# Kernel tuning notes

Measured on AMD Instinct MI355X. Metric: run time of the kernel, lower is better.

The kernel has to match this reference:

```python
import jax, jax.numpy as jnp
import numpy as np

B, L, NW, H, HID, E, NL, DL = 32, 1024, 512, 768, 384, 4, 12, 128


def setup_inputs() -> dict:
    key = jax.random.key(0)
    ks = jax.random.split(key, 16)
    f = lambda k, s: jax.random.normal(k, s, dtype=jnp.float32) * 0.02
    z = lambda s: jnp.zeros(s, jnp.float32)
    return {
        "token_embs": jax.random.normal(ks[0], (B, L, H), dtype=jnp.float32),
        "word_maps": jnp.sort(jax.random.randint(ks[1], (B, L), 0, NW), axis=-1),
        "lang_ids": jax.random.randint(ks[2], (B,), 0, NL),
        # BiLSTM params (PyTorch gate order i,f,g,o packed along dim 0)
        "Wih_f": f(ks[3], (4 * HID, H)), "Whh_f": f(ks[4], (4 * HID, HID)),
        "bih_f": z((4 * HID,)), "bhh_f": z((4 * HID,)),
        "Wih_b": f(ks[5], (4 * HID, H)), "Whh_b": f(ks[6], (4 * HID, HID)),
        "bih_b": z((4 * HID,)), "bhh_b": z((4 * HID,)),
        "proj_W": f(ks[7], (H, 2 * HID)), "proj_b": z((H,)),
        "lang_table": f(ks[8], (NL, DL)),
        "gate_W1": f(ks[9], (H, H + DL)), "gate_b1": z((H,)),
        "gate_W2": f(ks[10], (E, H)), "gate_b2": z((E,)),
        # stacked expert heads: row i is expert i's (H,1) linear
        "ef_W": f(ks[11], (E, H)), "ef_b": z((E,)),
        "ed_W": f(ks[12], (E, H)), "ed_b": z((E,)),
    }


def _seg_mean(embs, wmap):
    # embs: [L, H], wmap: [L] -> [NW, H] per-word mean of subword embeddings
    sums = jax.ops.segment_sum(embs, wmap, num_segments=NW)
    cnt = jax.ops.segment_sum(jnp.ones(embs.shape[:1], embs.dtype), wmap, num_segments=NW)
    return sums / jnp.maximum(cnt, 1.0)[:, None]


def _lstm(x, Wih, Whh, bih, bhh, reverse):
    # x: [B, T, H] -> hidden states [B, T, HID]; gate order i,f,g,o
    def step(carry, xg):
        h, c = carry
        g = xg + h @ Whh.T + bhh
        i, fg, gg, o = jnp.split(g, 4, axis=-1)
        c = jax.nn.sigmoid(fg) * c + jax.nn.sigmoid(i) * jnp.tanh(gg)
        h = jax.nn.sigmoid(o) * jnp.tanh(c)
        return (h, c), h
    xg = jnp.swapaxes(x @ Wih.T + bih, 0, 1)  # [T, B, 4*HID], input proj hoisted
    init = (jnp.zeros((x.shape[0], Whh.shape[1]), x.dtype),) * 2
    _, hs = jax.lax.scan(step, init, xg, reverse=reverse)
    return jnp.swapaxes(hs, 0, 1)


def reference(token_embs, word_maps, lang_ids, Wih_f, Whh_f, bih_f, bhh_f,
              Wih_b, Whh_b, bih_b, bhh_b, proj_W, proj_b, lang_table,
              gate_W1, gate_b1, gate_W2, gate_b2, ef_W, ef_b, ed_W, ed_b):
    # subword -> word segment-mean pooling, batched
    word_embs = jax.vmap(_seg_mean)(token_embs, word_maps)          # [B, NW, H]
    hf = _lstm(word_embs, Wih_f, Whh_f, bih_f, bhh_f, False)        # [B, NW, HID]
    hb = _lstm(word_embs, Wih_b, Whh_b, bih_b, bhh_b, True)         # [B, NW, HID]
    seq = jnp.concatenate([hf, hb], axis=-1) @ proj_W.T + proj_b    # [B, NW, H]
    # dropout omitted (eval mode)
    gate_in = jnp.concatenate([token_embs[:, 0], lang_table[lang_ids]], axis=-1)  # [B, H+DL]
    gate = jax.nn.softmax(
        jax.nn.relu(gate_in @ gate_W1.T + gate_b1) @ gate_W2.T + gate_b2, axis=-1)  # [B, E]
    fix = jnp.einsum('bwe,be->bw', seq @ ef_W.T + ef_b, gate)       # [B, NW]
    dur = jnp.einsum('bwe,be->bw', seq @ ed_W.T + ed_b, gate)       # [B, NW]
    return (fix, dur)
```

## Files before the change

kernel.cpp:

```cpp
#include <hip/hip_runtime.h>
#include <stdint.h>

#define BB 32
#define LL 1024
#define NW 512
#define HH 768
#define HID 384
#define G4 1536
#define EE 4
#define DLL 128
#define GIN 896
#define CWG 12
#define WGC 32
#define HPAD 392

typedef __attribute__((ext_vector_type(8))) short short8;
typedef __attribute__((ext_vector_type(4))) float f32x4;
typedef __attribute__((ext_vector_type(4))) unsigned int u32x4;
typedef __attribute__((ext_vector_type(2))) unsigned int u32x2;

__device__ __forceinline__ float bf2f(short s){
  union { unsigned int u; float f; } v; v.u = ((unsigned int)(unsigned short)s) << 16; return v.f;
}
__device__ __forceinline__ short f2bf(float f){
  union { float f; unsigned int u; } v; v.f = f;
  unsigned int r = v.u + 0x7fffu + ((v.u >> 16) & 1u);
  return (short)(r >> 16);
}
__device__ __forceinline__ float sigm(float x){ return 1.f / (1.f + __expf(-x)); }
__device__ __forceinline__ float ftanh(float x){ float e = __expf(2.f * x); return 1.f - 2.f / (e + 1.f); }

__device__ __forceinline__ void gload16(const void* g, void* l){
  __builtin_amdgcn_global_load_lds(
      (const __attribute__((address_space(1))) unsigned int*)g,
      (__attribute__((address_space(3))) unsigned int*)l, 16, 0, 0);
}

__global__ void k_f2bf(const float* in, short* out, int n){
  int i = blockIdx.x * blockDim.x + threadIdx.x;
  int st = gridDim.x * blockDim.x;
  for (; i < n; i += st) out[i] = f2bf(in[i]);
}

__global__ __launch_bounds__(256) void k_segmean(const float* __restrict__ tok,
                                                 const int* __restrict__ wmap,
                                                 short* __restrict__ we_bf){
  int blk = blockIdx.x;
  int b = blk >> 9;
  int w = blk & 511;
  const int* m = wmap + b * LL;
  int lo = 0, hi = LL;
  while (lo < hi){ int mid = (lo + hi) >> 1; if (m[mid] < w) lo = mid + 1; else hi = mid; }
  int s = lo;
  int lo2 = s, hi2 = LL;
  while (lo2 < hi2){ int mid = (lo2 + hi2) >> 1; if (m[mid] <= w) lo2 = mid + 1; else hi2 = mid; }
  int e = lo2;
  float cnt = (float)(e - s);
  float denom = fmaxf(cnt, 1.f);
  for (int j = threadIdx.x; j < HH; j += 256){
    float acc = 0.f;
    for (int r = s; r < e; ++r) acc += tok[((size_t)b * LL + r) * HH + j];
    we_bf[((size_t)b * NW + w) * HH + j] = f2bf(acc / denom);
  }
}

__global__ __launch_bounds__(256) void k_gemm_bt(const short* __restrict__ Abf,
                                                 const short* __restrict__ Wbf,
                                                 const float* __restrict__ b1,
                                                 const float* __restrict__ b2,
                                                 float* __restrict__ Cf,
                                                 int M, int N, int K){
  __shared__ __attribute__((aligned(16))) short As[128 * 32];
  __shared__ __attribute__((aligned(16))) short Bs[128 * 32];
  int ntiles = N >> 7;
  int m0 = (blockIdx.x / ntiles) << 7;
  int n0 = (blockIdx.x % ntiles) << 7;
  int tid = threadIdx.x, lane = tid & 63, wv = tid >> 6;
  int wm = (wv >> 1) << 6, wn = (wv & 1) << 6;
  f32x4 acc[4][4] = {};
  for (int kk = 0; kk < K; kk += 32){
#pragma unroll
    for (int q = 0; q < 2; ++q){
      int e = q * 256 + tid;
      int row = e >> 2, col = (e & 3) << 3;
      gload16(Abf + (size_t)(m0 + row) * K + kk + col, As + e * 8);
      gload16(Wbf + (size_t)(n0 + row) * K + kk + col, Bs + e * 8);
    }
    __syncthreads();
    short8 af[4], bfr[4];
#pragma unroll
    for (int x = 0; x < 4; ++x){
      af[x]  = *(const short8*)(As + (wm + x * 16 + (lane & 15)) * 32 + ((lane >> 4) << 3));
      bfr[x] = *(const short8*)(Bs + (wn + x * 16 + (lane & 15)) * 32 + ((lane >> 4) << 3));
    }
#pragma unroll
    for (int x = 0; x < 4; ++x)
#pragma unroll
      for (int y = 0; y < 4; ++y)
        acc[x][y] = __builtin_amdgcn_mfma_f32_16x16x32_bf16(af[x], bfr[y], acc[x][y], 0, 0, 0);
    __syncthreads();
  }
#pragma unroll
  for (int x = 0; x < 4; ++x)
#pragma unroll
    for (int y = 0; y < 4; ++y)
#pragma unroll
      for (int i = 0; i < 4; ++i){
        int mm = m0 + wm + x * 16 + ((lane >> 4) << 2) + i;
        int nn = n0 + wn + y * 16 + (lane & 15);
        Cf[(size_t)mm * N + nn] = acc[x][y][i] + b1[nn] + b2[nn];
      }
}

__global__ __launch_bounds__(512) void k_lstm(const float* __restrict__ xg_f,
                                              const float* __restrict__ xg_b,
                                              const short* __restrict__ whh_f,
                                              const short* __restrict__ whh_b,
                                              unsigned int* __restrict__ hbuf,
                                              short* __restrict__ hcat){
  int bx = blockIdx.x;
  int dir = bx / CWG;
  int cg  = bx % CWG;
  int tid = threadIdx.x, lane = tid & 63, wv = tid >> 6;
  int q = lane >> 4, fr = lane & 15;
  int g = wv >> 1, nh = wv & 1;
  int jbase = g * HID + cg * WGC + nh * 16;
  const float* xg  = dir ? xg_b : xg_f;
  const short* whh = dir ? whh_b : whh_f;

  short8 bfrag[12];
  {
    const short* wr = whh + (size_t)(jbase + fr) * HID + q * 8;
#pragma unroll
    for (int ks = 0; ks < 12; ++ks) bfrag[ks] = *(const short8*)(wr + ks * 32);
  }

  __shared__ __attribute__((aligned(16))) short hs[2][16 * HPAD];
  __shared__ float pre[4][16][34];

  float cst0 = 0.f, cst1 = 0.f;
  int eb = tid >> 5, ecol = tid & 31;
  int sc = (tid & 31) * 12;
  unsigned int* hbD = hbuf + (size_t)dir * 2 * 2 * 16 * HID;

  float nxg[4];
  {
    int t0a = dir ? (NW - 1) : 0;
    const float* xp = xg + (size_t)t0a * G4 + jbase + fr;
#pragma unroll
    for (int i = 0; i < 4; ++i)
      nxg[i] = xp[(size_t)(q * 4 + i) * NW * G4];
  }
  u32x4 d0, d1, d2;
  const unsigned int* hp_sav = hbD;

  for (int tt = 0; tt < 2 * NW; ++tt){
    int X = tt & 1, t = tt >> 1;
    int t_act = dir ? (NW - 1 - t) : t;
    asm volatile("s_waitcnt vmcnt(0)" ::: "memory");
    __builtin_amdgcn_sched_barrier(0);
    if (t > 0){
      unsigned int expect = (unsigned int)t & 0xffffu;
      for (;;){
#define TAGBAD(dv) (((dv[0] ^ expect) | (dv[1] ^ expect) | (dv[2] ^ expect) | (dv[3] ^ expect)) & 0xffffu)
        unsigned int bad = TAGBAD(d0) | TAGBAD(d1) | TAGBAD(d2);
#undef TAGBAD
        if (__all(bad == 0)) break;
        __builtin_amdgcn_s_sleep(1);
        asm volatile("global_load_dwordx4 %0, %1, off sc0 sc1" : "=v"(d0) : "v"(hp_sav + 0) : "memory");
        asm volatile("global_load_dwordx4 %0, %1, off sc0 sc1" : "=v"(d1) : "v"(hp_sav + 4) : "memory");
        asm volatile("global_load_dwordx4 %0, %1, off sc0 sc1" : "=v"(d2) : "v"(hp_sav + 8) : "memory");
        asm volatile("s_waitcnt vmcnt(0)" ::: "memory");
        __builtin_amdgcn_sched_barrier(0);
      }
      unsigned int pk0 = (d0[0] >> 16) | (d0[1] & 0xffff0000u);
      unsigned int pk1 = (d0[2] >> 16) | (d0[3] & 0xffff0000u);
      unsigned int pk2 = (d1[0] >> 16) | (d1[1] & 0xffff0000u);
      unsigned int pk3 = (d1[2] >> 16) | (d1[3] & 0xffff0000u);
      unsigned int pk4 = (d2[0] >> 16) | (d2[1] & 0xffff0000u);
      unsigned int pk5 = (d2[2] >> 16) | (d2[3] & 0xffff0000u);
      short* dst = &hs[X][eb * HPAD + sc];
      u32x2 w0 = {pk0, pk1}, w1 = {pk2, pk3}, w2 = {pk4, pk5};
      *(u32x2*)(dst)     = w0;
      *(u32x2*)(dst + 4) = w1;
      *(u32x2*)(dst + 8) = w2;
      if (cg == 0){
        int tprev = dir ? (NW - t) : (t - 1);
        short* dh = hcat + ((size_t)(X * 16 + eb) * NW + tprev) * HH + dir * HID + sc;
        *(u32x2*)(dh)     = w0;
        *(u32x2*)(dh + 4) = w1;
        *(u32x2*)(dh + 8) = w2;
      }
    }
    asm volatile("s_waitcnt lgkmcnt(0)" ::: "memory");
    __builtin_amdgcn_s_barrier();
    __builtin_amdgcn_sched_barrier(0);
    f32x4 acc = {}, accB = {};
    if (t > 0){
      const short* hrow = &hs[X][fr * HPAD + q * 8];
#pragma unroll
      for (int ks = 0; ks < 6; ++ks)
        acc  = __builtin_amdgcn_mfma_f32_16x16x32_bf16(*(const short8*)(hrow + ks * 32), bfrag[ks], acc, 0, 0, 0);
#pragma unroll
      for (int ks = 6; ks < 12; ++ks)
        accB = __builtin_amdgcn_mfma_f32_16x16x32_bf16(*(const short8*)(hrow + ks * 32), bfrag[ks], accB, 0, 0, 0);
      acc += accB;
    }
#pragma unroll
    for (int i = 0; i < 4; ++i)
      pre[g][q * 4 + i][nh * 16 + fr] = acc[i] + nxg[i];
    __builtin_amdgcn_sched_barrier(0);
    if (tt + 1 < 2 * NW){
      int Xn = 1 - X, tn = X ? (t + 1) : t;
      int tna = dir ? (NW - 1 - tn) : tn;
      const float* xp = xg + ((size_t)(Xn * 16) * NW + tna) * G4 + jbase + fr;
#pragma unroll
      for (int i = 0; i < 4; ++i)
        nxg[i] = xp[(size_t)(q * 4 + i) * NW * G4];
      if (tn > 0){
        hp_sav = hbD + ((size_t)Xn * 2 + ((tn - 1) & 1)) * 16 * HID + eb * HID + sc;
        asm volatile("global_load_dwordx4 %0, %1, off sc0 sc1" : "=v"(d0) : "v"(hp_sav + 0) : "memory");
        asm volatile("global_load_dwordx4 %0, %1, off sc0 sc1" : "=v"(d1) : "v"(hp_sav + 4) : "memory");
        asm volatile("global_load_dwordx4 %0, %1, off sc0 sc1" : "=v"(d2) : "v"(hp_sav + 8) : "memory");
      }
    }
    asm volatile("s_waitcnt lgkmcnt(0)" ::: "memory");
    __builtin_amdgcn_s_barrier();
    __builtin_amdgcn_sched_barrier(0);
    float gi2 = pre[0][eb][ecol], gf2 = pre[1][eb][ecol];
    float gg2 = pre[2][eb][ecol], go2 = pre[3][eb][ecol];
    float c = X ? cst1 : cst0;
    c = sigm(gf2) * c + sigm(gi2) * ftanh(gg2);
    float h = sigm(go2) * ftanh(c);
    if (X) cst1 = c; else cst0 = c;
    unsigned int hv = (unsigned int)(unsigned short)f2bf(h);
    unsigned int wtag = (hv << 16) | ((unsigned int)(t + 1) & 0xffffu);
    unsigned int* hw = hbD + ((size_t)X * 2 + (t & 1)) * 16 * HID + eb * HID + cg * WGC + ecol;
    asm volatile("global_store_dword %0, %1, off sc0 sc1" :: "v"(hw), "v"(wtag) : "memory");
    if (t == NW - 1)
      hcat[((size_t)(X * 16 + eb) * NW + t_act) * HH + dir * HID + cg * WGC + ecol] = (short)hv;
  }
}

__global__ __launch_bounds__(256) void k_gate(const float* __restrict__ tok,
                                              const int* __restrict__ lids,
                                              const float* __restrict__ ltab,
                                              const float* __restrict__ W1,
                                              const float* __restrict__ b1v,
                                              const float* __restrict__ W2,
                                              const float* __restrict__ b2v,
                                              float* __restrict__ gate){
  __shared__ float gin[GIN];
  __shared__ float hid[HH];
  __shared__ float pr[EE];
  int b = blockIdx.x, tid = threadIdx.x;
  int lid = lids[b];
  for (int i = tid; i < GIN; i += 256)
    gin[i] = (i < HH) ? tok[(size_t)b * LL * HH + i] : ltab[lid * DLL + (i - HH)];
  __syncthreads();
  for (int j = tid; j < HH; j += 256){
    float a = b1v[j];
    const float* wr = W1 + (size_t)j * GIN;
    for (int k = 0; k < GIN; ++k) a += gin[k] * wr[k];
    hid[j] = fmaxf(a, 0.f);
  }
  __syncthreads();
  int wv = tid >> 6, lane = tid & 63;
  if (wv < EE){
    float p = 0.f;
    for (int k = lane; k < HH; k += 64) p += hid[k] * W2[wv * HH + k];
#pragma unroll
    for (int off = 32; off; off >>= 1) p += __shfl_down(p, off);
    if (lane == 0) pr[wv] = p + b2v[wv];
  }
  __syncthreads();
  if (tid == 0){
    float mx = fmaxf(fmaxf(pr[0], pr[1]), fmaxf(pr[2], pr[3]));
    float s = 0.f, ex[EE];
    for (int e2 = 0; e2 < EE; ++e2){ ex[e2] = __expf(pr[e2] - mx); s += ex[e2]; }
    for (int e2 = 0; e2 < EE; ++e2) gate[b * EE + e2] = ex[e2] / s;
  }
}

__global__ __launch_bounds__(256) void k_headpre(const float* __restrict__ efW,
                                                 const float* __restrict__ efb,
                                                 const float* __restrict__ edW,
                                                 const float* __restrict__ edb,
                                                 const float* __restrict__ projW,
                                                 const float* __restrict__ projb,
                                                 float* __restrict__ Acomb,
                                                 float* __restrict__ Ccomb){
  int head = blockIdx.x >> 2, e2 = blockIdx.x & 3, tid = threadIdx.x;
  const float* Wv = head ? edW : efW;
  const float* bv = head ? edb : efb;
  __shared__ float wrow[HH];
  for (int i = tid; i < HH; i += 256) wrow[i] = Wv[e2 * HH + i];
  __syncthreads();
  for (int c = tid; c < HH; c += 256){
    float a = 0.f;
    for (int h2 = 0; h2 < HH; ++h2) a += wrow[h2] * projW[(size_t)h2 * HH + c];
    Acomb[(head * 4 + e2) * HH + c] = a;
  }
  int wv = tid >> 6, lane = tid & 63;
  if (wv == 0){
    float p = 0.f;
    for (int k = lane; k < HH; k += 64) p += wrow[k] * projb[k];
#pragma unroll
    for (int off = 32; off; off >>= 1) p += __shfl_down(p, off);
    if (lane == 0) Ccomb[head * 4 + e2] = p + bv[e2];
  }
}

__global__ __launch_bounds__(256) void k_heads(const short* __restrict__ hcat,
                                               const float* __restrict__ Acomb,
                                               const float* __restrict__ Ccomb,
                                               const float* __restrict__ gate,
                                               float* __restrict__ outp){
  __shared__ float Al[8 * HH];
  int tid = threadIdx.x;
  for (int i = tid; i < 8 * HH; i += 256) Al[i] = Acomb[i];
  __syncthreads();
  int wv = tid >> 6, lane = tid & 63;
  int bw = blockIdx.x * 4 + wv;
  const short* hr = hcat + (size_t)bw * HH;
  float hv[12];
#pragma unroll
  for (int j = 0; j < 12; ++j) hv[j] = bf2f(hr[lane + 64 * j]);
  float dsum[8];
#pragma unroll
  for (int v = 0; v < 8; ++v){
    float p = 0.f;
#pragma unroll
    for (int j = 0; j < 12; ++j) p += hv[j] * Al[v * HH + lane + 64 * j];
#pragma unroll
    for (int off = 32; off; off >>= 1) p += __shfl_xor(p, off);
    dsum[v] = p;
  }
  if (lane == 0){
    int b = bw >> 9;
    float fx = 0.f, du = 0.f;
#pragma unroll
    for (int e2 = 0; e2 < 4; ++e2){
      float g = gate[b * 4 + e2];
      fx += g * (dsum[e2]     + Ccomb[e2]);
      du += g * (dsum[4 + e2] + Ccomb[4 + e2]);
    }
    outp[bw] = fx;
    outp[BB * NW + bw] = du;
  }
}

extern "C" void kernel_launch(void* const* d_in, const int* in_sizes, int n_in,
                              void* d_out, int out_size, void* d_ws, size_t ws_size,
                              hipStream_t stream){
  const float* tok   = (const float*)d_in[0];
  const int*   wmap  = (const int*)d_in[1];
  const int*   lids  = (const int*)d_in[2];
  const float* Wih_f = (const float*)d_in[3];
  const float* Whh_f = (const float*)d_in[4];
  const float* bih_f = (const float*)d_in[5];
  const float* bhh_f = (const float*)d_in[6];
  const float* Wih_b = (const float*)d_in[7];
  const float* Whh_b = (const float*)d_in[8];
  const float* bih_b = (const float*)d_in[9];
  const float* bhh_b = (const float*)d_in[10];
  const float* projW = (const float*)d_in[11];
  const float* projb = (const float*)d_in[12];
  const float* ltab  = (const float*)d_in[13];
  const float* gW1   = (const float*)d_in[14];
  const float* gb1   = (const float*)d_in[15];
  const float* gW2   = (const float*)d_in[16];
  const float* gb2   = (const float*)d_in[17];
  const float* efW   = (const float*)d_in[18];
  const float* efb   = (const float*)d_in[19];
  const float* edW   = (const float*)d_in[20];
  const float* edb   = (const float*)d_in[21];
  float* outp = (float*)d_out;

  char* ws = (char*)d_ws;
  size_t off = 0;
  auto alloc = [&](size_t bytes) -> char* {
    char* p = ws + off;
    off = (off + bytes + 255) & ~(size_t)255;
    return p;
  };
  short* we_bf   = (short*)alloc((size_t)BB * NW * HH * 2);
  short* wihf_bf = (short*)alloc((size_t)G4 * HH * 2);
  short* wihb_bf = (short*)alloc((size_t)G4 * HH * 2);
  short* whhf_bf = (short*)alloc((size_t)G4 * HID * 2);
  short* whhb_bf = (short*)alloc((size_t)G4 * HID * 2);
  float* xg_f    = (float*)alloc((size_t)BB * NW * G4 * 4);
  float* xg_b    = (float*)alloc((size_t)BB * NW * G4 * 4);
  short* hcat    = (short*)alloc((size_t)BB * NW * HH * 2);
  unsigned int* hbuf = (unsigned int*)alloc((size_t)2 * 2 * 2 * 16 * HID * 4);
  float* gateb   = (float*)alloc((size_t)BB * EE * 4);
  float* Acomb   = (float*)alloc((size_t)8 * HH * 4);
  float* Ccomb   = (float*)alloc((size_t)8 * 4);

  k_f2bf<<<1024, 256, 0, stream>>>(Wih_f, wihf_bf, G4 * HH);
  k_f2bf<<<1024, 256, 0, stream>>>(Wih_b, wihb_bf, G4 * HH);
  k_f2bf<<<512, 256, 0, stream>>>(Whh_f, whhf_bf, G4 * HID);
  k_f2bf<<<512, 256, 0, stream>>>(Whh_b, whhb_bf, G4 * HID);
  k_segmean<<<BB * NW, 256, 0, stream>>>(tok, wmap, we_bf);
  k_gemm_bt<<<(BB * NW / 128) * (G4 / 128), 256, 0, stream>>>(we_bf, wihf_bf, bih_f, bhh_f, xg_f, BB * NW, G4, HH);
  k_gemm_bt<<<(BB * NW / 128) * (G4 / 128), 256, 0, stream>>>(we_bf, wihb_bf, bih_b, bhh_b, xg_b, BB * NW, G4, HH);
  k_gate<<<BB, 256, 0, stream>>>(tok, lids, ltab, gW1, gb1, gW2, gb2, gateb);
  k_headpre<<<8, 256, 0, stream>>>(efW, efb, edW, edb, projW, projb, Acomb, Ccomb);
  k_lstm<<<2 * CWG, 512, 0, stream>>>(xg_f, xg_b, whhf_bf, whhb_bf, hbuf, hcat);
  k_heads<<<(BB * NW) / 4, 256, 0, stream>>>(hcat, Acomb, Ccomb, gateb, outp);
}
```

Before: 2.378 ms.

## Unroll LSTM recurrence over two batch halves with counted vmcnt prefetching

The LSTM recurrence loop is manually unrolled into two explicit half-steps, one per batch half (A/B), each with its own hidden-state buffer and x-gate registers. Global loads now go through inline asm, and partial s_waitcnt vmcnt counts replace the full vmcnt(0) drain, so that one half's h exchange and xg prefetch stay in flight while the other half computes. The final step skips the tagged exchange store and writes hcat directly. The cost is hand-maintained wait counts that must match the exact issue order; a wrong count could read data before it arrives.

New measurement: 2.075 ms. 1.15x faster.

```diff
diff --git a/kernel.cpp b/kernel.cpp
--- a/kernel.cpp
+++ b/kernel.cpp
@@ -112,6 +112,8 @@
       }
 }
 
+#define TAGBAD(dv) (((dv[0] ^ expect) | (dv[1] ^ expect) | (dv[2] ^ expect) | (dv[3] ^ expect)) & 0xffffu)
+
 __global__ __launch_bounds__(512) void k_lstm(const float* __restrict__ xg_f,
                                               const float* __restrict__ xg_b,
                                               const short* __restrict__ whh_f,
@@ -132,113 +134,208 @@
   {
     const short* wr = whh + (size_t)(jbase + fr) * HID + q * 8;
 #pragma unroll
-    for (int ks = 0; ks < 12; ++ks) bfrag[ks] = *(const short8*)(wr + ks * 32);
+    for (int ks = 0; ks < 12; ++ks)
+      asm volatile("global_load_dwordx4 %0, %1, off" : "=v"(bfrag[ks]) : "v"(wr + ks * 32) : "memory");
+    asm volatile("s_waitcnt vmcnt(0)" ::: "memory");
+    __builtin_amdgcn_sched_barrier(0);
   }
 
   __shared__ __attribute__((aligned(16))) short hs[2][16 * HPAD];
   __shared__ float pre[4][16][34];
 
-  float cst0 = 0.f, cst1 = 0.f;
+  float cA = 0.f, cB = 0.f;
   int eb = tid >> 5, ecol = tid & 31;
   int sc = (tid & 31) * 12;
   unsigned int* hbD = hbuf + (size_t)dir * 2 * 2 * 16 * HID;
-
-  float nxg[4];
+  const size_t RS = (size_t)NW * G4;
+
+  float xa0, xa1, xa2, xa3, xb0, xb1, xb2, xb3;
+  u32x4 dA0, dA1, dA2, dB0, dB1, dB2;
+
   {
-    int t0a = dir ? (NW - 1) : 0;
-    const float* xp = xg + (size_t)t0a * G4 + jbase + fr;
-#pragma unroll
-    for (int i = 0; i < 4; ++i)
-      nxg[i] = xp[(size_t)(q * 4 + i) * NW * G4];
-  }
-  u32x4 d0, d1, d2;
-  const unsigned int* hp_sav = hbD;
-
-  for (int tt = 0; tt < 2 * NW; ++tt){
-    int X = tt & 1, t = tt >> 1;
-    int t_act = dir ? (NW - 1 - t) : t;
-    asm volatile("s_waitcnt vmcnt(0)" ::: "memory");
-    __builtin_amdgcn_sched_barrier(0);
-    if (t > 0){
-      unsigned int expect = (unsigned int)t & 0xffffu;
+    int ta = dir ? (NW - 1) : 0;
+    const float* xpA = xg + (size_t)ta * G4 + jbase + fr;
+    asm volatile("global_load_dword %0, %1, off" : "=v"(xa0) : "v"(xpA + (size_t)(q*4+0)*RS) : "memory");
+    asm volatile("global_load_dword %0, %1, off" : "=v"(xa1) : "v"(xpA + (size_t)(q*4+1)*RS) : "memory");
+    asm volatile("global_load_dword %0, %1, off" : "=v"(xa2) : "v"(xpA + (size_t)(q*4+2)*RS) : "memory");
+    asm volatile("global_load_dword %0, %1, off" : "=v"(xa3) : "v"(xpA + (size_t)(q*4+3)*RS) : "memory");
+    const float* xpB = xpA + (size_t)16 * RS;
+    asm volatile("global_load_dword %0, %1, off" : "=v"(xb0) : "v"(xpB + (size_t)(q*4+0)*RS) : "memory");
+    asm volatile("global_load_dword %0, %1, off" : "=v"(xb1) : "v"(xpB + (size_t)(q*4+1)*RS) : "memory");
+    asm volatile("global_load_dword %0, %1, off" : "=v"(xb2) : "v"(xpB + (size_t)(q*4+2)*RS) : "memory");
+    asm volatile("global_load_dword %0, %1, off" : "=v"(xb3) : "v"(xpB + (size_t)(q*4+3)*RS) : "memory");
+  }
+
+  for (int j = 0; j < NW; ++j){
+    int t_act = dir ? (NW - 1 - j) : j;
+    if (j == 0) { asm volatile("s_waitcnt vmcnt(4)" ::: "memory"); }
+    else        { asm volatile("s_waitcnt vmcnt(5)" ::: "memory"); }
+    __builtin_amdgcn_sched_barrier(0);
+    if (j > 0){
+      unsigned int expect = (unsigned int)j & 0xffffu;
+      const unsigned int* hpr = hbD + (size_t)((j - 1) & 1) * 16 * HID + eb * HID + sc;
       for (;;){
-#define TAGBAD(dv) (((dv[0] ^ expect) | (dv[1] ^ expect) | (dv[2] ^ expect) | (dv[3] ^ expect)) & 0xffffu)
-        unsigned int bad = TAGBAD(d0) | TAGBAD(d1) | TAGBAD(d2);
-#undef TAGBAD
+        unsigned int bad = TAGBAD(dA0) | TAGBAD(dA1) | TAGBAD(dA2);
         if (__all(bad == 0)) break;
         __builtin_amdgcn_s_sleep(1);
-        asm volatile("global_load_dwordx4 %0, %1, off sc0 sc1" : "=v"(d0) : "v"(hp_sav + 0) : "memory");
-        asm volatile("global_load_dwordx4 %0, %1, off sc0 sc1" : "=v"(d1) : "v"(hp_sav + 4) : "memory");
-        asm volatile("global_load_dwordx4 %0, %1, off sc0 sc1" : "=v"(d2) : "v"(hp_sav + 8) : "memory");
+        asm volatile("global_load_dwordx4 %0, %1, off sc0 sc1" : "=v"(dA0) : "v"(hpr + 0) : "memory");
+        asm volatile("global_load_dwordx4 %0, %1, off sc0 sc1" : "=v"(dA1) : "v"(hpr + 4) : "memory");
+        asm volatile("global_load_dwordx4 %0, %1, off sc0 sc1" : "=v"(dA2) : "v"(hpr + 8) : "memory");
         asm volatile("s_waitcnt vmcnt(0)" ::: "memory");
         __builtin_amdgcn_sched_barrier(0);
       }
-      unsigned int pk0 = (d0[0] >> 16) | (d0[1] & 0xffff0000u);
-      unsigned int pk1 = (d0[2] >> 16) | (d0[3] & 0xffff0000u);
-      unsigned int pk2 = (d1[0] >> 16) | (d1[1] & 0xffff0000u);
-      unsigned int pk3 = (d1[2] >> 16) | (d1[3] & 0xffff0000u);
-      unsigned int pk4 = (d2[0] >> 16) | (d2[1] & 0xffff0000u);
-      unsigned int pk5 = (d2[2] >> 16) | (d2[3] & 0xffff0000u);
-      short* dst = &hs[X][eb * HPAD + sc];
+      unsigned int pk0 = (dA0[0] >> 16) | (dA0[1] & 0xffff0000u);
+      unsigned int pk1 = (dA0[2] >> 16) | (dA0[3] & 0xffff0000u);
+      unsigned int pk2 = (dA1[0] >> 16) | (dA1[1] & 0xffff0000u);
+      unsigned int pk3 = (dA1[2] >> 16) | (dA1[3] & 0xffff0000u);
+      unsigned int pk4 = (dA2[0] >> 16) | (dA2[1] & 0xffff0000u);
+      unsigned int pk5 = (dA2[2] >> 16) | (dA2[3] & 0xffff0000u);
       u32x2 w0 = {pk0, pk1}, w1 = {pk2, pk3}, w2 = {pk4, pk5};
+      short* dst = &hs[0][eb * HPAD + sc];
       *(u32x2*)(dst)     = w0;
       *(u32x2*)(dst + 4) = w1;
       *(u32x2*)(dst + 8) = w2;
       if (cg == 0){
-        int tprev = dir ? (NW - t) : (t - 1);
-        short* dh = hcat + ((size_t)(X * 16 + eb) * NW + tprev) * HH + dir * HID + sc;
-        *(u32x2*)(dh)     = w0;
-        *(u32x2*)(dh + 4) = w1;
-        *(u32x2*)(dh + 8) = w2;
+        int tprev = dir ? (NW - j) : (j - 1);
+        short* dh = hcat + ((size_t)eb * NW + tprev) * HH + dir * HID + sc;
+        asm volatile("global_store_dwordx2 %0, %1, off" :: "v"(dh),     "v"(w0) : "memory");
+        asm volatile("global_store_dwordx2 %0, %1, off" :: "v"(dh + 4), "v"(w1) : "memory");
+        asm volatile("global_store_dwordx2 %0, %1, off" :: "v"(dh + 8), "v"(w2) : "memory");
       }
     }
     asm volatile("s_waitcnt lgkmcnt(0)" ::: "memory");
     __builtin_amdgcn_s_barrier();
     __builtin_amdgcn_sched_barrier(0);
-    f32x4 acc = {}, accB = {};
-    if (t > 0){
-      const short* hrow = &hs[X][fr * HPAD + q * 8];
+    f32x4 acc = {}, acc2 = {};
+    if (j > 0){
+      const short* hrow = &hs[0][fr * HPAD + q * 8];
 #pragma unroll
       for (int ks = 0; ks < 6; ++ks)
         acc  = __builtin_amdgcn_mfma_f32_16x16x32_bf16(*(const short8*)(hrow + ks * 32), bfrag[ks], acc, 0, 0, 0);
 #pragma unroll
       for (int ks = 6; ks < 12; ++ks)
-        accB = __builtin_amdgcn_mfma_f32_16x16x32_bf16(*(const short8*)(hrow + ks * 32), bfrag[ks], accB, 0, 0, 0);
-      acc += accB;
-    }
-#pragma unroll
-    for (int i = 0; i < 4; ++i)
-      pre[g][q * 4 + i][nh * 16 + fr] = acc[i] + nxg[i];
-    __builtin_amdgcn_sched_barrier(0);
-    if (tt + 1 < 2 * NW){
-      int Xn = 1 - X, tn = X ? (t + 1) : t;
-      int tna = dir ? (NW - 1 - tn) : tn;
-      const float* xp = xg + ((size_t)(Xn * 16) * NW + tna) * G4 + jbase + fr;
-#pragma unroll
-      for (int i = 0; i < 4; ++i)
-        nxg[i] = xp[(size_t)(q * 4 + i) * NW * G4];
-      if (tn > 0){
-        hp_sav = hbD + ((size_t)Xn * 2 + ((tn - 1) & 1)) * 16 * HID + eb * HID + sc;
-        asm volatile("global_load_dwordx4 %0, %1, off sc0 sc1" : "=v"(d0) : "v"(hp_sav + 0) : "memory");
-        asm volatile("global_load_dwordx4 %0, %1, off sc0 sc1" : "=v"(d1) : "v"(hp_sav + 4) : "memory");
-        asm volatile("global_load_dwordx4 %0, %1, off sc0 sc1" : "=v"(d2) : "v"(hp_sav + 8) : "memory");
-      }
+        acc2 = __builtin_amdgcn_mfma_f32_16x16x32_bf16(*(const short8*)(hrow + ks * 32), bfrag[ks], acc2, 0, 0, 0);
+      acc += acc2;
+    }
+    pre[g][q*4+0][nh*16+fr] = acc[0] + xa0;
+    pre[g][q*4+1][nh*16+fr] = acc[1] + xa1;
+    pre[g][q*4+2][nh*16+fr] = acc[2] + xa2;
+    pre[g][q*4+3][nh*16+fr] = acc[3] + xa3;
+    if (j > 0){
+      const unsigned int* hpn = hbD + ((size_t)2 + ((j - 1) & 1)) * 16 * HID + eb * HID + sc;
+      asm volatile("global_load_dwordx4 %0, %1, off sc0 sc1" : "=v"(dB0) : "v"(hpn + 0) : "memory");
+      asm volatile("global_load_dwordx4 %0, %1, off sc0 sc1" : "=v"(dB1) : "v"(hpn + 4) : "memory");
+      asm volatile("global_load_dwordx4 %0, %1, off sc0 sc1" : "=v"(dB2) : "v"(hpn + 8) : "memory");
+    }
+    if (j + 1 < NW){
+      int ta2 = dir ? (NW - 2 - j) : (j + 1);
+      const float* xp2 = xg + (size_t)ta2 * G4 + jbase + fr;
+      asm volatile("global_load_dword %0, %1, off" : "=v"(xa0) : "v"(xp2 + (size_t)(q*4+0)*RS) : "memory");
+      asm volatile("global_load_dword %0, %1, off" : "=v"(xa1) : "v"(xp2 + (size_t)(q*4+1)*RS) : "memory");
+      asm volatile("global_load_dword %0, %1, off" : "=v"(xa2) : "v"(xp2 + (size_t)(q*4+2)*RS) : "memory");
+      asm volatile("global_load_dword %0, %1, off" : "=v"(xa3) : "v"(xp2 + (size_t)(q*4+3)*RS) : "memory");
     }
     asm volatile("s_waitcnt lgkmcnt(0)" ::: "memory");
     __builtin_amdgcn_s_barrier();
     __builtin_amdgcn_sched_barrier(0);
-    float gi2 = pre[0][eb][ecol], gf2 = pre[1][eb][ecol];
-    float gg2 = pre[2][eb][ecol], go2 = pre[3][eb][ecol];
-    float c = X ? cst1 : cst0;
-    c = sigm(gf2) * c + sigm(gi2) * ftanh(gg2);
-    float h = sigm(go2) * ftanh(c);
-    if (X) cst1 = c; else cst0 = c;
-    unsigned int hv = (unsigned int)(unsigned short)f2bf(h);
-    unsigned int wtag = (hv << 16) | ((unsigned int)(t + 1) & 0xffffu);
-    unsigned int* hw = hbD + ((size_t)X * 2 + (t & 1)) * 16 * HID + eb * HID + cg * WGC + ecol;
-    asm volatile("global_store_dword %0, %1, off sc0 sc1" :: "v"(hw), "v"(wtag) : "memory");
-    if (t == NW - 1)
-      hcat[((size_t)(X * 16 + eb) * NW + t_act) * HH + dir * HID + cg * WGC + ecol] = (short)hv;
+    {
+      float gi2 = pre[0][eb][ecol], gf2 = pre[1][eb][ecol];
+      float gg2 = pre[2][eb][ecol], go2 = pre[3][eb][ecol];
+      cA = sigm(gf2) * cA + sigm(gi2) * ftanh(gg2);
+      float h = sigm(go2) * ftanh(cA);
+      unsigned int hv = (unsigned int)(unsigned short)f2bf(h);
+      if (j < NW - 1){
+        unsigned int wtag = (hv << 16) | ((unsigned int)(j + 1) & 0xffffu);
+        unsigned int* hw = hbD + (size_t)(j & 1) * 16 * HID + eb * HID + cg * WGC + ecol;
+        asm volatile("global_store_dword %0, %1, off sc0 sc1" :: "v"(hw), "v"(wtag) : "memory");
+      } else {
+        short* hc = hcat + ((size_t)eb * NW + t_act) * HH + dir * HID + cg * WGC + ecol;
+        asm volatile("global_store_short %0, %1, off" :: "v"(hc), "v"(hv) : "memory");
+      }
+    }
+    if (j == NW - 1) { asm volatile("s_waitcnt vmcnt(1)" ::: "memory"); }
+    else             { asm volatile("s_waitcnt vmcnt(5)" ::: "memory"); }
+    __builtin_amdgcn_sched_barrier(0);
+    if (j > 0){
+      unsigned int expect = (unsigned int)j & 0xffffu;
+      const unsigned int* hpr = hbD + ((size_t)2 + ((j - 1) & 1)) * 16 * HID + eb * HID + sc;
+      for (;;){
+        unsigned int bad = TAGBAD(dB0) | TAGBAD(dB1) | TAGBAD(dB2);
+        if (__all(bad == 0)) break;
+        __builtin_amdgcn_s_sleep(1);
+        asm volatile("global_load_dwordx4 %0, %1, off sc0 sc1" : "=v"(dB0) : "v"(hpr + 0) : "memory");
+        asm volatile("global_load_dwordx4 %0, %1, off sc0 sc1" : "=v"(dB1) : "v"(hpr + 4) : "memory");
+        asm volatile("global_load_dwordx4 %0, %1, off sc0 sc1" : "=v"(dB2) : "v"(hpr + 8) : "memory");
+        asm volatile("s_waitcnt vmcnt(0)" ::: "memory");
+        __builtin_amdgcn_sched_barrier(0);
+      }
+      unsigned int pk0 = (dB0[0] >> 16) | (dB0[1] & 0xffff0000u);
+      unsigned int pk1 = (dB0[2] >> 16) | (dB0[3] & 0xffff0000u);
+      unsigned int pk2 = (dB1[0] >> 16) | (dB1[1] & 0xffff0000u);
+      unsigned int pk3 = (dB1[2] >> 16) | (dB1[3] & 0xffff0000u);
+      unsigned int pk4 = (dB2[0] >> 16) | (dB2[1] & 0xffff0000u);
+      unsigned int pk5 = (dB2[2] >> 16) | (dB2[3] & 0xffff0000u);
+      u32x2 w0 = {pk0, pk1}, w1 = {pk2, pk3}, w2 = {pk4, pk5};
+      short* dst = &hs[1][eb * HPAD + sc];
+      *(u32x2*)(dst)     = w0;
+      *(u32x2*)(dst + 4) = w1;
+      *(u32x2*)(dst + 8) = w2;
+      if (cg == 0){
+        int tprev = dir ? (NW - j) : (j - 1);
+        short* dh = hcat + ((size_t)(16 + eb) * NW + tprev) * HH + dir * HID + sc;
+        asm volatile("global_store_dwordx2 %0, %1, off" :: "v"(dh),     "v"(w0) : "memory");
+        asm volatile("global_store_dwordx2 %0, %1, off" :: "v"(dh + 4), "v"(w1) : "memory");
+        asm volatile("global_store_dwordx2 %0, %1, off" :: "v"(dh + 8), "v"(w2) : "memory");
+      }
+    }
+    asm volatile("s_waitcnt lgkmcnt(0)" ::: "memory");
+    __builtin_amdgcn_s_barrier();
+    __builtin_amdgcn_sched_barrier(0);
+    f32x4 accb = {}, accb2 = {};
+    if (j > 0){
+      const short* hrow = &hs[1][fr * HPAD + q * 8];
+#pragma unroll
+      for (int ks = 0; ks < 6; ++ks)
+        accb  = __builtin_amdgcn_mfma_f32_16x16x32_bf16(*(const short8*)(hrow + ks * 32), bfrag[ks], accb, 0, 0, 0);
+#pragma unroll
+      for (int ks = 6; ks < 12; ++ks)
+        accb2 = __builtin_amdgcn_mfma_f32_16x16x32_bf16(*(const short8*)(hrow + ks * 32), bfrag[ks], accb2, 0, 0, 0);
+      accb += accb2;
+    }
+    pre[g][q*4+0][nh*16+fr] = accb[0] + xb0;
+    pre[g][q*4+1][nh*16+fr] = accb[1] + xb1;
+    pre[g][q*4+2][nh*16+fr] = accb[2] + xb2;
+    pre[g][q*4+3][nh*16+fr] = accb[3] + xb3;
+    if (j + 1 < NW){
+      const unsigned int* hpn = hbD + (size_t)(j & 1) * 16 * HID + eb * HID + sc;
+      asm volatile("global_load_dwordx4 %0, %1, off sc0 sc1" : "=v"(dA0) : "v"(hpn + 0) : "memory");
+      asm volatile("global_load_dwordx4 %0, %1, off sc0 sc1" : "=v"(dA1) : "v"(hpn + 4) : "memory");
+      asm volatile("global_load_dwordx4 %0, %1, off sc0 sc1" : "=v"(dA2) : "v"(hpn + 8) : "memory");
+      int ta2 = dir ? (NW - 2 - j) : (j + 1);
+      const float* xp2 = xg + (size_t)ta2 * G4 + jbase + fr + (size_t)16 * RS;
+      asm volatile("global_load_dword %0, %1, off" : "=v"(xb0) : "v"(xp2 + (size_t)(q*4+0)*RS) : "memory");
+      asm volatile("global_load_dword %0, %1, off" : "=v"(xb1) : "v"(xp2 + (size_t)(q*4+1)*RS) : "memory");
+      asm volatile("global_load_dword %0, %1, off" : "=v"(xb2) : "v"(xp2 + (size_t)(q*4+2)*RS) : "memory");
+      asm volatile("global_load_dword %0, %1, off" : "=v"(xb3) : "v"(xp2 + (size_t)(q*4+3)*RS) : "memory");
+    }
+    asm volatile("s_waitcnt lgkmcnt(0)" ::: "memory");
+    __builtin_amdgcn_s_barrier();
+    __builtin_amdgcn_sched_barrier(0);
+    {
+      float gi2 = pre[0][eb][ecol], gf2 = pre[1][eb][ecol];
+      float gg2 = pre[2][eb][ecol], go2 = pre[3][eb][ecol];
+      cB = sigm(gf2) * cB + sigm(gi2) * ftanh(gg2);
+      float h = sigm(go2) * ftanh(cB);
+      unsigned int hv = (unsigned int)(unsigned short)f2bf(h);
+      if (j < NW - 1){
+        unsigned int wtag = (hv << 16) | ((unsigned int)(j + 1) & 0xffffu);
+        unsigned int* hw = hbD + ((size_t)2 + (j & 1)) * 16 * HID + eb * HID + cg * WGC + ecol;
+        asm volatile("global_store_dword %0, %1, off sc0 sc1" :: "v"(hw), "v"(wtag) : "memory");
+      } else {
+        short* hc = hcat + ((size_t)(16 + eb) * NW + t_act) * HH + dir * HID + cg * WGC + ecol;
+        asm volatile("global_store_short %0, %1, off" :: "v"(hc), "v"(hv) : "memory");
+      }
+    }
   }
 }
 
```
